# Kernel optimization log

Hardware: AMD Instinct MI355X
Metric: run time of the kernel (lower is better)

## Reference

```python
import jax, jax.numpy as jnp
import numpy as np

N_NODES = 100000
N_EDGES = 1600000
IN_DIM = 128
HID = 32
HEADS = 4
NUM_CLASS = 2


def setup_inputs() -> dict:
    key = jax.random.key(0)
    ks = jax.random.split(key, 10)
    x = jax.random.normal(ks[0], (N_NODES, IN_DIM), dtype=jnp.float32)
    edge_index = jax.random.randint(ks[1], (2, N_EDGES), 0, N_NODES, dtype=jnp.int64)
    s_in = 1.0 / np.sqrt(IN_DIM)
    s_h = 1.0 / np.sqrt(HEADS * HID)
    return {
        "x": x,
        "edge_index": edge_index,
        "W1": jax.random.normal(ks[2], (HEADS * HID, IN_DIM), dtype=jnp.float32) * s_in,
        "att_src1": jax.random.normal(ks[3], (HEADS, HID), dtype=jnp.float32) * s_in,
        "att_dst1": jax.random.normal(ks[4], (HEADS, HID), dtype=jnp.float32) * s_in,
        "b1": jnp.zeros((HEADS * HID,), dtype=jnp.float32),
        "W2": jax.random.normal(ks[5], (NUM_CLASS, HEADS * HID), dtype=jnp.float32) * s_h,
        "att_src2": jax.random.normal(ks[6], (1, NUM_CLASS), dtype=jnp.float32) * s_h,
        "att_dst2": jax.random.normal(ks[7], (1, NUM_CLASS), dtype=jnp.float32) * s_h,
        "b2": jnp.zeros((NUM_CLASS,), dtype=jnp.float32),
    }


def gat_conv(x, src, dst, W, att_src, att_dst, b, n):
    """PyG-style GATConv (self-loops already included in src/dst)."""
    H, C = att_src.shape
    h = (x @ W.T).reshape(n, H, C)                      # [N,H,C]
    a_s = jnp.einsum('nhc,hc->nh', h, att_src)           # [N,H]
    a_d = jnp.einsum('nhc,hc->nh', h, att_dst)           # [N,H]
    e = jax.nn.leaky_relu(a_s[src] + a_d[dst], 0.2)      # [E,H]
    m = jax.ops.segment_max(e, dst, num_segments=n)      # per-dst max
    m = jnp.where(jnp.isfinite(m), m, 0.0)
    ex = jnp.exp(e - m[dst])
    denom = jax.ops.segment_sum(ex, dst, num_segments=n)
    alpha = ex / (denom[dst] + 1e-16)                    # segment softmax
    out = jax.ops.segment_sum(h[src] * alpha[..., None], dst, num_segments=n)
    return out.reshape(n, H * C) + b


def reference(x, edge_index, W1, att_src1, att_dst1, b1, W2, att_src2, att_dst2, b2):
    n = x.shape[0]
    loops = jnp.arange(n, dtype=edge_index.dtype)
    ei = jnp.concatenate([edge_index, jnp.stack([loops, loops])], axis=1)
    src, dst = ei[0], ei[1]
    h = gat_conv(x, src, dst, W1, att_src1, att_dst1, b1, n)
    h = jax.nn.leaky_relu(h, 0.01)  # F.leaky_relu default slope
    # F.dropout with p=0.0 -> identity
    out = gat_conv(h, src, dst, W2, att_src2, att_dst2, b2, n)
    return jax.nn.log_softmax(out, axis=1)
```

## Files before the change

### kernel.cpp

```cpp
#include <hip/hip_runtime.h>

#define NN 100000
#define NE 1600000
#define NTOT (NN + NE)
#define NB 782
#define ACHUNK 2048
#define NCH 782
#define BCAP 3072

typedef __attribute__((ext_vector_type(8))) short bf16x8;
typedef __attribute__((ext_vector_type(4))) float f32x4;

static __device__ __forceinline__ float blo(unsigned int u) {
  union { unsigned int i; float f; } v; v.i = u << 16; return v.f;
}
static __device__ __forceinline__ float bhi(unsigned int u) {
  union { unsigned int i; float f; } v; v.i = u & 0xffff0000u; return v.f;
}
static __device__ __forceinline__ unsigned short f2bf(float f) {
  union { float f; unsigned int i; } v; v.f = f;
  unsigned int i = v.i;
  i += 0x7fffu + ((i >> 16) & 1u);
  return (unsigned short)(i >> 16);
}

__global__ __launch_bounds__(512) void kb_hist(const int* __restrict__ ei,
                                               int* __restrict__ cntMat) {
  __shared__ int h[NB];
  int tid = threadIdx.x, blk = blockIdx.x;
  int e0 = blk * ACHUNK;
  int n = min(ACHUNK, NE - e0);
  for (int i = tid; i < NB; i += 512) h[i] = 0;
  __syncthreads();
  for (int i = tid; i < n; i += 512) atomicAdd(&h[ei[NE + e0 + i] >> 7], 1);
  __syncthreads();
  for (int i = tid; i < NB; i += 512) cntMat[blk * NB + i] = h[i];
}

__global__ void kb_colscan(int* __restrict__ cntMat, int* __restrict__ bucketCnt) {
  int b = blockIdx.x;
  int lane = threadIdx.x;
  int carry = 0;
  for (int base = 0; base < NCH; base += 64) {
    int idx = base + lane;
    int v = (idx < NCH) ? cntMat[idx * NB + b] : 0;
    int x = v;
#pragma unroll
    for (int d = 1; d < 64; d <<= 1) {
      int y = __shfl_up(x, d, 64);
      if (lane >= d) x += y;
    }
    if (idx < NCH) cntMat[idx * NB + b] = carry + x - v;
    carry += __shfl(x, 63, 64);
  }
  if (lane == 0) bucketCnt[b] = carry;
}

__global__ void kb_scan(const int* __restrict__ bucketCnt, int* __restrict__ pairOffset) {
  int lane = threadIdx.x;
  int c[13];
  int run = 0;
  int idx0 = lane * 13;
#pragma unroll
  for (int k = 0; k < 13; ++k) {
    int idx = idx0 + k;
    int v = (idx < NB) ? bucketCnt[idx] : 0;
    c[k] = run;
    run += v;
  }
  int x = run;
#pragma unroll
  for (int d = 1; d < 64; d <<= 1) {
    int y = __shfl_up(x, d, 64);
    if (lane >= d) x += y;
  }
  int laneoff = x - run;
#pragma unroll
  for (int k = 0; k < 13; ++k) {
    int idx = idx0 + k;
    if (idx <= NB) pairOffset[idx] = laneoff + c[k];
  }
}

__global__ __launch_bounds__(512) void kb_scatA(const int* __restrict__ ei,
                                                const int* __restrict__ pairOffset,
                                                const int* __restrict__ cntMat,
                                                int* __restrict__ pair) {
  __shared__ int lcnt[NB + 1];
  __shared__ int gbase[NB];
  __shared__ int lcur[NB];
  __shared__ int stage[ACHUNK];
  int tid = threadIdx.x, blk = blockIdx.x;
  int e0 = blk * ACHUNK;
  int n = min(ACHUNK, NE - e0);
  for (int i = tid; i <= NB; i += 512) lcnt[i] = 0;
  __syncthreads();
  for (int i = tid; i < n; i += 512) atomicAdd(&lcnt[ei[NE + e0 + i] >> 7], 1);
  __syncthreads();
  if (tid < 64) {
    int c[13];
    int run = 0;
    int idx0 = tid * 13;
#pragma unroll
    for (int k = 0; k < 13; ++k) {
      int idx = idx0 + k;
      int v = (idx < NB) ? lcnt[idx] : 0;
      c[k] = run;
      run += v;
    }
    int x = run;
#pragma unroll
    for (int d = 1; d < 64; d <<= 1) {
      int y = __shfl_up(x, d, 64);
      if (tid >= d) x += y;
    }
    int laneoff = x - run;
#pragma unroll
    for (int k = 0; k < 13; ++k) {
      int idx = idx0 + k;
      if (idx <= NB) lcnt[idx] = laneoff + c[k];
    }
  }
  __syncthreads();
  for (int b = tid; b < NB; b += 512) {
    gbase[b] = pairOffset[b] + cntMat[blk * NB + b];
    lcur[b] = lcnt[b];
  }
  __syncthreads();
  for (int i = tid; i < n; i += 512) {
    int s = ei[e0 + i], d = ei[NE + e0 + i];
    int b = d >> 7;
    int p = atomicAdd(&lcur[b], 1);
    stage[p] = (s << 7) | (d & 127);
  }
  __syncthreads();
  for (int b = tid; b < NB; b += 512) {
    int base = lcnt[b], cnt = lcnt[b + 1] - base, g = gbase[b];
    for (int k = 0; k < cnt; ++k) pair[g + k] = stage[base + k];
  }
}

__global__ __launch_bounds__(256) void kb_binB(const int* __restrict__ pair,
                                               const int* __restrict__ pairOffset,
                                               int* __restrict__ rowptr,
                                               int* __restrict__ col) {
  __shared__ int cnt[128];
  __shared__ int cur[128];
  __shared__ int stage[BCAP];
  int tid = threadIdx.x;
  int b = blockIdx.x;
  int dbase = b << 7;
  int nd = min(128, NN - dbase);
  int pbeg = pairOffset[b], m = pairOffset[b + 1] - pbeg;
  int cbase = pbeg + dbase;
  if (tid < 128) cnt[tid] = 0;
  __syncthreads();
  for (int i = tid; i < m; i += 256) atomicAdd(&cnt[pair[pbeg + i] & 127], 1);
  __syncthreads();
  if (tid < 64) {
    int i0 = 2 * tid, i1 = 2 * tid + 1;
    int v0 = cnt[i0] + (i0 < nd ? 1 : 0);
    int v1 = cnt[i1] + (i1 < nd ? 1 : 0);
    int run = v0 + v1;
    int x = run;
#pragma unroll
    for (int d = 1; d < 64; d <<= 1) {
      int y = __shfl_up(x, d, 64);
      if (tid >= d) x += y;
    }
    int e0 = x - run;
    int e1 = e0 + v0;
    if (i0 < nd) { rowptr[dbase + i0] = cbase + e0; stage[e0] = dbase + i0; cur[i0] = e0 + 1; }
    else cur[i0] = e0;
    if (i1 < nd) { rowptr[dbase + i1] = cbase + e1; stage[e1] = dbase + i1; cur[i1] = e1 + 1; }
    else cur[i1] = e1;
  }
  if (b == NB - 1 && tid == 0) rowptr[NN] = NTOT;
  __syncthreads();
  for (int i = tid; i < m; i += 256) {
    int p = pair[pbeg + i];
    int pos = atomicAdd(&cur[p & 127], 1);
    stage[pos] = p >> 7;
  }
  __syncthreads();
  int tot = m + nd;
  for (int i = tid; i < tot; i += 256) col[cbase + i] = stage[i];
}

__global__ void k_cvtW(const float* __restrict__ W1, unsigned short* __restrict__ Whp,
                       unsigned short* __restrict__ Wlp) {
  int i = blockIdx.x * 256 + threadIdx.x;
  if (i < 128 * 128) {
    int row = i >> 7, k = i & 127;
    int ot = row >> 4, r16 = row & 15;
    int c = k >> 5, quad = (k >> 3) & 3, j = k & 7;
    int dst = ((ot * 4 + c) * 64 + quad * 16 + r16) * 8 + j;
    float v = W1[i];
    unsigned short h = f2bf(v);
    Whp[dst] = h;
    Wlp[dst] = f2bf(v - blo((unsigned int)h));
  }
}

__global__ __launch_bounds__(256, 5) void k_gemm1(
    const float* __restrict__ x, const unsigned short* __restrict__ Whp,
    const unsigned short* __restrict__ Wlp, const float* __restrict__ asrc,
    const float* __restrict__ adst, unsigned short* __restrict__ h1b,
    float4* __restrict__ as1, float4* __restrict__ ad1) {
  __shared__ float xs[4][16 * 129];
  int wid = threadIdx.x >> 6, lane = threadIdx.x & 63;
  int tile = blockIdx.x * 4 + wid;
  if (tile >= NN / 16) tile = NN / 16 - 1;
  int r16 = lane & 15, quad = lane >> 4;
  const float4* xg = (const float4*)(x + (size_t)tile * 16 * 128);
  {
    int half = lane >> 5, l32 = lane & 31;
#pragma unroll
    for (int i = 0; i < 8; ++i) {
      int row = i * 2 + half;
      float4 v = xg[row * 32 + l32];
      float* dp = &xs[wid][row * 129 + l32 * 4];
      dp[0] = v.x; dp[1] = v.y; dp[2] = v.z; dp[3] = v.w;
    }
  }
  bf16x8 bh[4], bl[4];
  const float* xr = &xs[wid][r16 * 129 + quad * 8];
#pragma unroll
  for (int c = 0; c < 4; ++c) {
#pragma unroll
    for (int j = 0; j < 8; ++j) {
      float v = xr[c * 32 + j];
      union { float f; unsigned int i; } u; u.f = v;
      bh[c][j] = (short)(u.i >> 16);
      union { float f; unsigned int i; } l; l.f = v - bhi(u.i);
      bl[c][j] = (short)(l.i >> 16);
    }
  }
  float asp[4] = {0.f, 0.f, 0.f, 0.f};
  float adp[4] = {0.f, 0.f, 0.f, 0.f};
  int node = tile * 16 + r16;
#pragma unroll
  for (int ot = 0; ot < 8; ++ot) {
    f32x4 acc = {0.f, 0.f, 0.f, 0.f};
#pragma unroll
    for (int c = 0; c < 4; ++c) {
      const bf16x8 wh = *(const bf16x8*)(Whp + ((size_t)(ot * 4 + c) * 64 + lane) * 8);
      const bf16x8 wl = *(const bf16x8*)(Wlp + ((size_t)(ot * 4 + c) * 64 + lane) * 8);
      acc = __builtin_amdgcn_mfma_f32_16x16x32_bf16(wh, bh[c], acc, 0, 0, 0);
      acc = __builtin_amdgcn_mfma_f32_16x16x32_bf16(wl, bh[c], acc, 0, 0, 0);
      acc = __builtin_amdgcn_mfma_f32_16x16x32_bf16(wh, bl[c], acc, 0, 0, 0);
    }
    float4 sa = *(const float4*)(asrc + ot * 16 + quad * 4);
    float4 da = *(const float4*)(adst + ot * 16 + quad * 4);
    const int hh = ot >> 1;
    asp[hh] += acc[0] * sa.x + acc[1] * sa.y + acc[2] * sa.z + acc[3] * sa.w;
    adp[hh] += acc[0] * da.x + acc[1] * da.y + acc[2] * da.z + acc[3] * da.w;
    unsigned short* o = h1b + (size_t)node * 128 + ot * 16 + quad * 4;
    unsigned int p01 = (unsigned int)f2bf(acc[0]) | ((unsigned int)f2bf(acc[1]) << 16);
    unsigned int p23 = (unsigned int)f2bf(acc[2]) | ((unsigned int)f2bf(acc[3]) << 16);
    *(uint2*)o = make_uint2(p01, p23);
  }
#pragma unroll
  for (int h = 0; h < 4; ++h) {
    asp[h] += __shfl_xor(asp[h], 16, 64);
    asp[h] += __shfl_xor(asp[h], 32, 64);
    adp[h] += __shfl_xor(adp[h], 16, 64);
    adp[h] += __shfl_xor(adp[h], 32, 64);
  }
  if (lane < 16) {
    as1[node] = make_float4(asp[0], asp[1], asp[2], asp[3]);
    ad1[node] = make_float4(adp[0], adp[1], adp[2], adp[3]);
  }
}

__global__ __launch_bounds__(256, 6) void k_agg1(
    const unsigned short* __restrict__ h1b, const float* __restrict__ as1,
    const float* __restrict__ ad1, const int* __restrict__ rowptr,
    const int* __restrict__ col, const float* __restrict__ b1,
    const float* __restrict__ W2, const float* __restrict__ asrc2,
    const float* __restrict__ adst2, float4* __restrict__ node2) {
  int wid = threadIdx.x >> 6, lane = threadIdx.x & 63;
  int grp = lane >> 4, l16 = lane & 15;
  int node = blockIdx.x * 16 + wid * 4 + grp;
  int head = l16 >> 2;
  float ad = ad1[node * 4 + head];
  int beg = rowptr[node], deg = rowptr[node + 1] - beg;
  const uint4* h1q = (const uint4*)h1b;
  float acc[8] = {0.f, 0.f, 0.f, 0.f, 0.f, 0.f, 0.f, 0.f};
  float wsum = 0.f;
  int j = 0;
  while (__ballot(j < deg)) {
    bool a[8]; int s[8];
#pragma unroll
    for (int k = 0; k < 8; ++k) {
      a[k] = (j + k) < deg;
      s[k] = a[k] ? col[beg + j + k] : 0;
    }
    float e[8]; uint4 u[8];
#pragma unroll
    for (int k = 0; k < 8; ++k) e[k] = as1[s[k] * 4 + head] + ad;
#pragma unroll
    for (int k = 0; k < 8; ++k) u[k] = h1q[(size_t)s[k] * 16 + l16];
#pragma unroll
    for (int k = 0; k < 8; ++k) {
      float t = e[k];
      t = (t < 0.f) ? 0.2f * t : t;
      float w = a[k] ? __expf(fminf(t, 80.f)) : 0.f;
      wsum += w;
      acc[0] += w * blo(u[k].x); acc[1] += w * bhi(u[k].x);
      acc[2] += w * blo(u[k].y); acc[3] += w * bhi(u[k].y);
      acc[4] += w * blo(u[k].z); acc[5] += w * bhi(u[k].z);
      acc[6] += w * blo(u[k].w); acc[7] += w * bhi(u[k].w);
    }
    j += 8;
  }
  float inv = 1.f / (wsum + 1e-16f);
  int cb = l16 * 8;
  float h[8];
#pragma unroll
  for (int t = 0; t < 8; ++t) {
    float v = acc[t] * inv + b1[cb + t];
    h[t] = (v < 0.f) ? 0.01f * v : v;
  }
  float p0 = 0.f, p1 = 0.f;
#pragma unroll
  for (int t = 0; t < 8; ++t) {
    p0 += h[t] * W2[cb + t];
    p1 += h[t] * W2[128 + cb + t];
  }
  p0 += __shfl_xor(p0, 1, 64); p0 += __shfl_xor(p0, 2, 64);
  p0 += __shfl_xor(p0, 4, 64); p0 += __shfl_xor(p0, 8, 64);
  p1 += __shfl_xor(p1, 1, 64); p1 += __shfl_xor(p1, 2, 64);
  p1 += __shfl_xor(p1, 4, 64); p1 += __shfl_xor(p1, 8, 64);
  if (l16 == 0) {
    float as2 = p0 * asrc2[0] + p1 * asrc2[1];
    float ad2 = p0 * adst2[0] + p1 * adst2[1];
    node2[node] = make_float4(p0, p1, as2, ad2);
  }
}

__global__ void k_agg2(const float4* __restrict__ node2, const int* __restrict__ rowptr,
                       const int* __restrict__ col, const float* __restrict__ b2,
                       float2* __restrict__ out) {
  int t = blockIdx.x * 256 + threadIdx.x;
  int node = t >> 3, sub = t & 7;
  if (node >= NN) return;
  float ad2 = node2[node].w;
  int beg = rowptr[node], end = rowptr[node + 1];
  float den = 0.f, a0 = 0.f, a1 = 0.f;
  for (int j = beg + sub; j < end; j += 8) {
    int s = col[j];
    float4 sv = node2[s];
    float e = sv.z + ad2;
    e = (e < 0.f) ? 0.2f * e : e;
    float w = __expf(fminf(e, 80.f));
    den += w;
    a0 += w * sv.x;
    a1 += w * sv.y;
  }
#pragma unroll
  for (int d = 1; d < 8; d <<= 1) {
    den += __shfl_xor(den, d, 64);
    a0 += __shfl_xor(a0, d, 64);
    a1 += __shfl_xor(a1, d, 64);
  }
  if (sub == 0) {
    float inv = 1.f / (den + 1e-16f);
    float o0 = a0 * inv + b2[0];
    float o1 = a1 * inv + b2[1];
    float m = fmaxf(o0, o1);
    float lse = m + __logf(__expf(o0 - m) + __expf(o1 - m));
    out[node] = make_float2(o0 - lse, o1 - lse);
  }
}

extern "C" void kernel_launch(void* const* d_in, const int* in_sizes, int n_in,
                              void* d_out, int out_size, void* d_ws, size_t ws_size,
                              hipStream_t stream) {
  const float* x     = (const float*)d_in[0];
  const int*   ei    = (const int*)d_in[1];
  const float* W1    = (const float*)d_in[2];
  const float* asrc1 = (const float*)d_in[3];
  const float* adst1 = (const float*)d_in[4];
  const float* b1    = (const float*)d_in[5];
  const float* W2    = (const float*)d_in[6];
  const float* asrc2 = (const float*)d_in[7];
  const float* adst2 = (const float*)d_in[8];
  const float* b2    = (const float*)d_in[9];
  float2* out = (float2*)d_out;

  int* rowptr     = (int*)d_ws;
  int* col        = rowptr + 100352;
  int* pair       = col + 1700096;
  int* cntMat     = pair + 1600000;
  int* bucketCnt  = cntMat + 611584;
  int* pairOffset = bucketCnt + 1024;
  unsigned short* h1b = (unsigned short*)(pairOffset + 1024);
  float*  as1  = (float*)(h1b + (size_t)NN * 128);
  float*  ad1  = as1 + NN * 4;
  float4* node2 = (float4*)(ad1 + NN * 4);
  unsigned short* W1h = (unsigned short*)(node2 + NN);
  unsigned short* W1l = W1h + 16384;

  kb_hist<<<NCH, 512, 0, stream>>>(ei, cntMat);
  kb_colscan<<<NB, 64, 0, stream>>>(cntMat, bucketCnt);
  kb_scan<<<1, 64, 0, stream>>>(bucketCnt, pairOffset);
  kb_scatA<<<NCH, 512, 0, stream>>>(ei, pairOffset, cntMat, pair);
  kb_binB<<<NB, 256, 0, stream>>>(pair, pairOffset, rowptr, col);
  k_cvtW<<<64, 256, 0, stream>>>(W1, W1h, W1l);
  k_gemm1<<<(NN / 16 + 3) / 4, 256, 0, stream>>>(x, W1h, W1l, asrc1, adst1, h1b,
                                                 (float4*)as1, (float4*)ad1);
  k_agg1<<<NN / 16, 256, 0, stream>>>(h1b, as1, ad1, rowptr, col, b1, W2, asrc2, adst2, node2);
  k_agg2<<<(NN * 8 + 255) / 256, 256, 0, stream>>>(node2, rowptr, col, b2, out);
}
```

Before: 257.6 us.

## Co-schedule GEMM with CSR build kernels and fold weight conversion into histogram

```diff
diff --git a/kernel.cpp b/kernel.cpp
--- a/kernel.cpp
+++ b/kernel.cpp
@@ -4,9 +4,10 @@
 #define NE 1600000
 #define NTOT (NN + NE)
 #define NB 782
-#define ACHUNK 2048
-#define NCH 782
+#define ACHUNK 4096
+#define NCH 391
 #define BCAP 3072
+#define G1SPLIT 940
 
 typedef __attribute__((ext_vector_type(8))) short bf16x8;
 typedef __attribute__((ext_vector_type(4))) float f32x4;
@@ -24,17 +25,35 @@
   return (unsigned short)(i >> 16);
 }
 
-__global__ __launch_bounds__(512) void kb_hist(const int* __restrict__ ei,
-                                               int* __restrict__ cntMat) {
+__global__ __launch_bounds__(512) void k_histcvt(const int* __restrict__ ei,
+                                                 int* __restrict__ cntMat,
+                                                 const float* __restrict__ W1,
+                                                 unsigned short* __restrict__ Whp,
+                                                 unsigned short* __restrict__ Wlp) {
   __shared__ int h[NB];
-  int tid = threadIdx.x, blk = blockIdx.x;
-  int e0 = blk * ACHUNK;
-  int n = min(ACHUNK, NE - e0);
-  for (int i = tid; i < NB; i += 512) h[i] = 0;
-  __syncthreads();
-  for (int i = tid; i < n; i += 512) atomicAdd(&h[ei[NE + e0 + i] >> 7], 1);
-  __syncthreads();
-  for (int i = tid; i < NB; i += 512) cntMat[blk * NB + i] = h[i];
+  int tid = threadIdx.x;
+  if (blockIdx.x < NCH) {
+    int blk = blockIdx.x;
+    int e0 = blk * ACHUNK;
+    int n = min(ACHUNK, NE - e0);
+    for (int i = tid; i < NB; i += 512) h[i] = 0;
+    __syncthreads();
+    for (int i = tid; i < n; i += 512) atomicAdd(&h[ei[NE + e0 + i] >> 7], 1);
+    __syncthreads();
+    for (int i = tid; i < NB; i += 512) cntMat[blk * NB + i] = h[i];
+  } else {
+    int i = (blockIdx.x - NCH) * 512 + tid;
+    if (i < 128 * 128) {
+      int row = i >> 7, k = i & 127;
+      int ot = row >> 4, r16 = row & 15;
+      int c = k >> 5, quad = (k >> 3) & 3, j = k & 7;
+      int dst = ((ot * 4 + c) * 64 + quad * 16 + r16) * 8 + j;
+      float v = W1[i];
+      unsigned short hh = f2bf(v);
+      Whp[dst] = hh;
+      Wlp[dst] = f2bf(v - blo((unsigned int)hh));
+    }
+  }
 }
 
 __global__ void kb_colscan(int* __restrict__ cntMat, int* __restrict__ bucketCnt) {
@@ -82,15 +101,16 @@
   }
 }
 
-__global__ __launch_bounds__(512) void kb_scatA(const int* __restrict__ ei,
-                                                const int* __restrict__ pairOffset,
-                                                const int* __restrict__ cntMat,
-                                                int* __restrict__ pair) {
-  __shared__ int lcnt[NB + 1];
-  __shared__ int gbase[NB];
-  __shared__ int lcur[NB];
-  __shared__ int stage[ACHUNK];
-  int tid = threadIdx.x, blk = blockIdx.x;
+static __device__ __forceinline__ void scat_role(char* smem, int blk,
+                                                 const int* __restrict__ ei,
+                                                 const int* __restrict__ pairOffset,
+                                                 const int* __restrict__ cntMat,
+                                                 int* __restrict__ pair) {
+  int* lcnt = (int*)smem;
+  int* gbase = lcnt + (NB + 1);
+  int* lcur = gbase + NB;
+  int* stage = lcur + NB;
+  int tid = threadIdx.x;
   int e0 = blk * ACHUNK;
   int n = min(ACHUNK, NE - e0);
   for (int i = tid; i <= NB; i += 512) lcnt[i] = 0;
@@ -140,15 +160,15 @@
   }
 }
 
-__global__ __launch_bounds__(256) void kb_binB(const int* __restrict__ pair,
-                                               const int* __restrict__ pairOffset,
-                                               int* __restrict__ rowptr,
-                                               int* __restrict__ col) {
-  __shared__ int cnt[128];
-  __shared__ int cur[128];
-  __shared__ int stage[BCAP];
+static __device__ __forceinline__ void bin_role(char* smem, int b,
+                                                const int* __restrict__ pair,
+                                                const int* __restrict__ pairOffset,
+                                                int* __restrict__ rowptr,
+                                                int* __restrict__ col) {
+  int* cnt = (int*)smem;
+  int* cur = cnt + 128;
+  int* stage = cur + 128;
   int tid = threadIdx.x;
-  int b = blockIdx.x;
   int dbase = b << 7;
   int nd = min(128, NN - dbase);
   int pbeg = pairOffset[b], m = pairOffset[b + 1] - pbeg;
@@ -187,30 +207,15 @@
   for (int i = tid; i < tot; i += 256) col[cbase + i] = stage[i];
 }
 
-__global__ void k_cvtW(const float* __restrict__ W1, unsigned short* __restrict__ Whp,
-                       unsigned short* __restrict__ Wlp) {
-  int i = blockIdx.x * 256 + threadIdx.x;
-  if (i < 128 * 128) {
-    int row = i >> 7, k = i & 127;
-    int ot = row >> 4, r16 = row & 15;
-    int c = k >> 5, quad = (k >> 3) & 3, j = k & 7;
-    int dst = ((ot * 4 + c) * 64 + quad * 16 + r16) * 8 + j;
-    float v = W1[i];
-    unsigned short h = f2bf(v);
-    Whp[dst] = h;
-    Wlp[dst] = f2bf(v - blo((unsigned int)h));
-  }
-}
-
-__global__ __launch_bounds__(256, 5) void k_gemm1(
+static __device__ __forceinline__ void gemm_role(char* smem, int gblk,
     const float* __restrict__ x, const unsigned short* __restrict__ Whp,
     const unsigned short* __restrict__ Wlp, const float* __restrict__ asrc,
     const float* __restrict__ adst, unsigned short* __restrict__ h1b,
     float4* __restrict__ as1, float4* __restrict__ ad1) {
-  __shared__ float xs[4][16 * 129];
   int wid = threadIdx.x >> 6, lane = threadIdx.x & 63;
-  int tile = blockIdx.x * 4 + wid;
+  int tile = gblk * 4 + wid;
   if (tile >= NN / 16) tile = NN / 16 - 1;
+  float* xs = (float*)smem + wid * (16 * 129);
   int r16 = lane & 15, quad = lane >> 4;
   const float4* xg = (const float4*)(x + (size_t)tile * 16 * 128);
   {
@@ -219,12 +224,12 @@
     for (int i = 0; i < 8; ++i) {
       int row = i * 2 + half;
       float4 v = xg[row * 32 + l32];
-      float* dp = &xs[wid][row * 129 + l32 * 4];
+      float* dp = &xs[row * 129 + l32 * 4];
       dp[0] = v.x; dp[1] = v.y; dp[2] = v.z; dp[3] = v.w;
     }
   }
   bf16x8 bh[4], bl[4];
-  const float* xr = &xs[wid][r16 * 129 + quad * 8];
+  const float* xr = &xs[r16 * 129 + quad * 8];
 #pragma unroll
   for (int c = 0; c < 4; ++c) {
 #pragma unroll
@@ -271,6 +276,37 @@
     as1[node] = make_float4(asp[0], asp[1], asp[2], asp[3]);
     ad1[node] = make_float4(adp[0], adp[1], adp[2], adp[3]);
   }
+}
+
+__global__ __launch_bounds__(512) void k_scatgemm(
+    const int* __restrict__ ei, const int* __restrict__ pairOffset,
+    const int* __restrict__ cntMat, int* __restrict__ pair,
+    const float* __restrict__ x, const unsigned short* __restrict__ Whp,
+    const unsigned short* __restrict__ Wlp, const float* __restrict__ asrc,
+    const float* __restrict__ adst, unsigned short* __restrict__ h1b,
+    float4* __restrict__ as1, float4* __restrict__ ad1) {
+  __shared__ __align__(16) char smem[33024];
+  if (blockIdx.x < NCH) {
+    scat_role(smem, blockIdx.x, ei, pairOffset, cntMat, pair);
+    return;
+  }
+  if (threadIdx.x >= 256) return;
+  gemm_role(smem, blockIdx.x - NCH, x, Whp, Wlp, asrc, adst, h1b, as1, ad1);
+}
+
+__global__ __launch_bounds__(256) void k_bingemm(
+    const int* __restrict__ pair, const int* __restrict__ pairOffset,
+    int* __restrict__ rowptr, int* __restrict__ col,
+    const float* __restrict__ x, const unsigned short* __restrict__ Whp,
+    const unsigned short* __restrict__ Wlp, const float* __restrict__ asrc,
+    const float* __restrict__ adst, unsigned short* __restrict__ h1b,
+    float4* __restrict__ as1, float4* __restrict__ ad1) {
+  __shared__ __align__(16) char smem[33024];
+  if (blockIdx.x < NB) {
+    bin_role(smem, blockIdx.x, pair, pairOffset, rowptr, col);
+    return;
+  }
+  gemm_role(smem, G1SPLIT + (int)blockIdx.x - NB, x, Whp, Wlp, asrc, adst, h1b, as1, ad1);
 }
 
 __global__ __launch_bounds__(256, 6) void k_agg1(
@@ -393,7 +429,7 @@
   int* col        = rowptr + 100352;
   int* pair       = col + 1700096;
   int* cntMat     = pair + 1600000;
-  int* bucketCnt  = cntMat + 611584;
+  int* bucketCnt  = cntMat + 305792;
   int* pairOffset = bucketCnt + 1024;
   unsigned short* h1b = (unsigned short*)(pairOffset + 1024);
   float*  as1  = (float*)(h1b + (size_t)NN * 128);
@@ -402,14 +438,15 @@
   unsigned short* W1h = (unsigned short*)(node2 + NN);
   unsigned short* W1l = W1h + 16384;
 
-  kb_hist<<<NCH, 512, 0, stream>>>(ei, cntMat);
+  k_histcvt<<<NCH + 32, 512, 0, stream>>>(ei, cntMat, W1, W1h, W1l);
   kb_colscan<<<NB, 64, 0, stream>>>(cntMat, bucketCnt);
   kb_scan<<<1, 64, 0, stream>>>(bucketCnt, pairOffset);
-  kb_scatA<<<NCH, 512, 0, stream>>>(ei, pairOffset, cntMat, pair);
-  kb_binB<<<NB, 256, 0, stream>>>(pair, pairOffset, rowptr, col);
-  k_cvtW<<<64, 256, 0, stream>>>(W1, W1h, W1l);
-  k_gemm1<<<(NN / 16 + 3) / 4, 256, 0, stream>>>(x, W1h, W1l, asrc1, adst1, h1b,
-                                                 (float4*)as1, (float4*)ad1);
+  k_scatgemm<<<NCH + G1SPLIT, 512, 0, stream>>>(ei, pairOffset, cntMat, pair,
+                                                x, W1h, W1l, asrc1, adst1, h1b,
+                                                (float4*)as1, (float4*)ad1);
+  k_bingemm<<<NB + (1563 - G1SPLIT), 256, 0, stream>>>(pair, pairOffset, rowptr, col,
+                                                       x, W1h, W1l, asrc1, adst1, h1b,
+                                                       (float4*)as1, (float4*)ad1);
   k_agg1<<<NN / 16, 256, 0, stream>>>(h1b, as1, ad1, rowptr, col, b1, W2, asrc2, adst2, node2);
   k_agg2<<<(NN * 8 + 255) / 256, 256, 0, stream>>>(node2, rowptr, col, b2, out);
 }
```

After: 246.9 us. 4.2% less time.
